# Kernel tuning notes

Hardware: AMD Instinct MI355X
Metric: run time of the kernel (lower is better)

Reference implementation:

```python
import jax, jax.numpy as jnp
import numpy as np

TGT, BSZ, E, H = 2048, 4, 1024, 16
HD = E // H


def setup_inputs() -> dict:
    key = jax.random.key(0)
    ks = jax.random.split(key, 9)
    s = 1.0 / np.sqrt(E)
    return {
        "query": jax.random.normal(ks[0], (TGT, BSZ, E), jnp.float32),
        "wq": jax.random.normal(ks[1], (E, E), jnp.float32) * s,
        "bq": jax.random.normal(ks[2], (E,), jnp.float32) * 0.01,
        "wk": jax.random.normal(ks[3], (E, E), jnp.float32) * s,
        "bk": jax.random.normal(ks[4], (E,), jnp.float32) * 0.01,
        "wv": jax.random.normal(ks[5], (E, E), jnp.float32) * s,
        "bv": jax.random.normal(ks[6], (E,), jnp.float32) * 0.01,
        "wo": jax.random.normal(ks[7], (E, E), jnp.float32) * s,
        "bo": jax.random.normal(ks[8], (E,), jnp.float32) * 0.01,
    }


def reference(query, wq, bq, wk, bk, wv, bv, wo, bo):
    tgt_len, bsz, embed_dim = query.shape
    scaling = HD ** (-0.5)
    # self-attention: q,k,v all projected from query (torch Linear: x @ W.T + b)
    q = (query @ wq.T + bq) * scaling
    k = query @ wk.T + bk
    v = query @ wv.T + bv
    # [T, B, E] -> [B, H, T, HD]
    def split_heads(x):
        return x.reshape(tgt_len, bsz, H, HD).transpose(1, 2, 0, 3)
    qh, kh, vh = split_heads(q), split_heads(k), split_heads(v)
    # attention scores [B, H, Tq, Tk]
    scores = jnp.einsum("bhqd,bhkd->bhqk", qh, kh)
    attn = jax.nn.softmax(scores, axis=-1)
    ctx = jnp.einsum("bhqk,bhkd->bhqd", attn, vh)  # [B, H, T, HD]
    ctx = ctx.transpose(2, 0, 1, 3).reshape(tgt_len, bsz, embed_dim)
    out = ctx @ wo.T + bo
    # need_weights=True default: average attn weights over heads [B, Tq, Tk]
    avg_attn = attn.mean(axis=1)
    return out, avg_attn
```

## Files before the change

kernel.cpp:

```cpp
#include <hip/hip_runtime.h>
#include <cstdint>
#include <cstddef>

typedef _Float16 f16;
typedef f16   f16x4 __attribute__((ext_vector_type(4)));
typedef f16   f16x8 __attribute__((ext_vector_type(8)));
typedef float f32x4 __attribute__((ext_vector_type(4)));

#define MFMA16x32(a, b, c) __builtin_amdgcn_mfma_f32_16x16x32_f16((a), (b), (c), 0, 0, 0)
#define MFMA16x16(a, b, c) __builtin_amdgcn_mfma_f32_16x16x16f16((a), (b), (c), 0, 0, 0)

__device__ __forceinline__ void gload_lds16(const void* g, void* l) {
    __builtin_amdgcn_global_load_lds(
        (const __attribute__((address_space(1))) unsigned int*)g,
        (__attribute__((address_space(3))) unsigned int*)l, 16, 0, 0);
}

__global__ void cvt_f32_f16(const float* __restrict__ in, f16* __restrict__ out, int n8) {
    int i = blockIdx.x * blockDim.x + threadIdx.x;
    if (i >= n8) return;
    const float4 a = ((const float4*)in)[i * 2];
    const float4 b = ((const float4*)in)[i * 2 + 1];
    f16x8 o;
    o[0] = (f16)a.x; o[1] = (f16)a.y; o[2] = (f16)a.z; o[3] = (f16)a.w;
    o[4] = (f16)b.x; o[5] = (f16)b.y; o[6] = (f16)b.z; o[7] = (f16)b.w;
    *(f16x8*)(out + (size_t)i * 8) = o;
}

__global__ __launch_bounds__(256, 3)
void gemm_qkv(const f16* __restrict__ A, const f16* __restrict__ B,
              const float* __restrict__ bq, const float* __restrict__ bk,
              const float* __restrict__ bv,
              f16* __restrict__ q_sp, f16* __restrict__ k_sp, f16* __restrict__ v_sp)
{
    __shared__ f16 Al[128 * 32];
    __shared__ f16 Bl[128 * 32];
    const int tid = threadIdx.x, lane = tid & 63, w = tid >> 6;
    const int wm = w >> 1, wn = w & 1;
    const int m0 = blockIdx.y * 128, n0 = blockIdx.x * 128;
    const int l15 = lane & 15, lh = lane >> 4;

    f32x4 acc[4][4] = {};

    const int c0 = w, c1 = w + 4;
    const int srow0 = c0 * 16 + (lane >> 2);
    const int srow1 = c1 * 16 + (lane >> 2);
    const int scol = (lane & 3) * 8;

    for (int k0 = 0; k0 < 1024; k0 += 32) {
        gload_lds16(A + (size_t)(m0 + srow0) * 1024 + k0 + scol, &Al[c0 * 512]);
        gload_lds16(A + (size_t)(m0 + srow1) * 1024 + k0 + scol, &Al[c1 * 512]);
        gload_lds16(B + (size_t)(n0 + srow0) * 1024 + k0 + scol, &Bl[c0 * 512]);
        gload_lds16(B + (size_t)(n0 + srow1) * 1024 + k0 + scol, &Bl[c1 * 512]);
        __syncthreads();
        f16x8 af[4], bf[4];
        #pragma unroll
        for (int i = 0; i < 4; ++i) {
            af[i] = *(const f16x8*)&Al[(wm * 64 + i * 16 + l15) * 32 + lh * 8];
            bf[i] = *(const f16x8*)&Bl[(wn * 64 + i * 16 + l15) * 32 + lh * 8];
        }
        #pragma unroll
        for (int i = 0; i < 4; ++i)
            #pragma unroll
            for (int j = 0; j < 4; ++j)
                acc[i][j] = MFMA16x32(af[i], bf[j], acc[i][j]);
        __syncthreads();
    }

    const int seg = n0 >> 10;
    const float* bias = (seg == 0) ? bq : (seg == 1) ? bk : bv;
    f16* dst = (seg == 0) ? q_sp : (seg == 1) ? k_sp : v_sp;
    const float scale = (seg == 0) ? 0.18033688011112042f : 1.0f;

    #pragma unroll
    for (int j = 0; j < 4; ++j) {
        const int n = n0 + wn * 64 + j * 16 + l15;
        const int e = n & 1023, hh = e >> 6, d = e & 63;
        const float bsv = bias[e];
        #pragma unroll
        for (int i = 0; i < 4; ++i) {
            #pragma unroll
            for (int r = 0; r < 4; ++r) {
                const int m = m0 + wm * 64 + i * 16 + lh * 4 + r;
                const int t = m >> 2, bb = m & 3;
                dst[((size_t)(bb * 16 + hh) * 2048 + t) * 64 + d] =
                    (f16)((acc[i][j][r] + bsv) * scale);
            }
        }
    }
}

__global__ __launch_bounds__(256)
void vpack(const f16* __restrict__ v_sp, f16* __restrict__ vf_) {
    __shared__ f16 L[16 * 64];
    const int nt = blockIdx.x, bh = blockIdx.y;
    const int tid = threadIdx.x;
    const f16* src = v_sp + ((size_t)bh * 2048 + nt * 16) * 64;
    if (tid < 128)
        *(f16x8*)&L[tid * 8] = *(const f16x8*)&src[tid * 8];
    __syncthreads();
    const int lane = tid >> 2, dt = tid & 3;
    const int l15 = lane & 15, lh = lane >> 4;
    f16x4 o;
    #pragma unroll
    for (int r = 0; r < 4; ++r) o[r] = L[(lh * 4 + r) * 64 + dt * 16 + l15];
    *(f16x4*)&vf_[((size_t)bh * 128 + nt) * 1024 + tid * 4] = o;
}

__global__ __launch_bounds__(512, 2)
void attn_kernel(const f16* __restrict__ q_s, const f16* __restrict__ k_s,
                 const f16* __restrict__ v_f, f16* __restrict__ ctx,
                 float* __restrict__ avg_out)
{
    __shared__ float Oacc[2][1024];
    __shared__ float sumL[8][16];

    const int tid = threadIdx.x;
    const int lane = tid & 63;
    const int w = tid >> 6;
    const int b = blockIdx.y;
    const int t0 = blockIdx.x * 16;
    const int l15 = lane & 15, lh = lane >> 4;

    f16x4 avgv[16] = {};

    Oacc[0][tid] = 0.f; Oacc[0][tid + 512] = 0.f;
    Oacc[1][tid] = 0.f; Oacc[1][tid + 512] = 0.f;

    for (int h = 0; h < 16; ++h) {
        const f16* Qh  = q_s + ((size_t)(b * 16 + h) * 2048 + t0) * 64;
        const f16* Kh  = k_s + (size_t)(b * 16 + h) * 2048 * 64 + (size_t)w * 256 * 64;
        const f16* Vfh = v_f + (size_t)(b * 16 + h) * 131072 + (size_t)w * 16 * 1024;

        const f16x8 qf0 = *(const f16x8*)(Qh + l15 * 64 + lh * 8);
        const f16x8 qf1 = *(const f16x8*)(Qh + l15 * 64 + 32 + lh * 8);

        f16x4 t[16];
        float rsum = 0.f;
        #pragma unroll
        for (int nt = 0; nt < 16; ++nt) {
            const f16* kp = Kh + (size_t)(nt * 16 + l15) * 64 + lh * 8;
            const f16x8 kf0 = *(const f16x8*)(kp);
            const f16x8 kf1 = *(const f16x8*)(kp + 32);
            f32x4 s = {0.f, 0.f, 0.f, 0.f};
            s = MFMA16x32(kf0, qf0, s);
            s = MFMA16x32(kf1, qf1, s);
            const float e0 = __builtin_amdgcn_exp2f(s[0]);
            const float e1 = __builtin_amdgcn_exp2f(s[1]);
            const float e2 = __builtin_amdgcn_exp2f(s[2]);
            const float e3 = __builtin_amdgcn_exp2f(s[3]);
            rsum += (e0 + e1) + (e2 + e3);
            f16x4 tv;
            tv[0] = (f16)e0; tv[1] = (f16)e1; tv[2] = (f16)e2; tv[3] = (f16)e3;
            t[nt] = tv;
        }
        rsum += __shfl_xor(rsum, 16);
        rsum += __shfl_xor(rsum, 32);
        if (lane < 16) sumL[w][lane] = rsum;
        __syncthreads();

        Oacc[(h + 1) & 1][tid] = 0.f;
        Oacc[(h + 1) & 1][tid + 512] = 0.f;

        float total = 0.f;
        #pragma unroll
        for (int ww = 0; ww < 8; ++ww) total += sumL[ww][l15];
        const f16 hinv = (f16)(1.f / total);
        f16x4 hv; hv[0] = hinv; hv[1] = hinv; hv[2] = hinv; hv[3] = hinv;

        f32x4 o0 = {}, o1 = {}, o2 = {}, o3 = {};
        #pragma unroll
        for (int nt = 0; nt < 16; ++nt) {
            const f16x4 tn = t[nt] * hv;
            avgv[nt] += tn;
            const f16* vp = Vfh + nt * 1024 + lane * 16;
            const f16x8 vab = *(const f16x8*)(vp);
            const f16x8 vcd = *(const f16x8*)(vp + 8);
            const f16x4 va = __builtin_shufflevector(vab, vab, 0, 1, 2, 3);
            const f16x4 vb = __builtin_shufflevector(vab, vab, 4, 5, 6, 7);
            const f16x4 vc = __builtin_shufflevector(vcd, vcd, 0, 1, 2, 3);
            const f16x4 vd = __builtin_shufflevector(vcd, vcd, 4, 5, 6, 7);
            o0 = MFMA16x16(tn, va, o0);
            o1 = MFMA16x16(tn, vb, o1);
            o2 = MFMA16x16(tn, vc, o2);
            o3 = MFMA16x16(tn, vd, o3);
        }
        float* Ob = Oacc[h & 1];
        #pragma unroll
        for (int r = 0; r < 4; ++r) {
            const int rowb = (lh * 4 + r) * 64;
            atomicAdd(&Ob[rowb +      l15], o0[r]);
            atomicAdd(&Ob[rowb + 16 + l15], o1[r]);
            atomicAdd(&Ob[rowb + 32 + l15], o2[r]);
            atomicAdd(&Ob[rowb + 48 + l15], o3[r]);
        }
        __syncthreads();

        #pragma unroll
        for (int jj = 0; jj < 2; ++jj) {
            const int idx = tid + jj * 512;
            const int q = idx >> 6, d = idx & 63;
            ctx[((size_t)(t0 + q) * 4 + b) * 1024 + h * 64 + d] = (f16)Ob[idx];
        }
    }

    const float s16 = 1.f / 16.f;
    float* ao = avg_out + ((size_t)b * 2048 + t0 + l15) * 2048 + w * 256 + lh * 4;
    #pragma unroll
    for (int nt = 0; nt < 16; ++nt) {
        float4 v;
        v.x = (float)avgv[nt][0] * s16; v.y = (float)avgv[nt][1] * s16;
        v.z = (float)avgv[nt][2] * s16; v.w = (float)avgv[nt][3] * s16;
        *(float4*)(ao + nt * 16) = v;
    }
}

__global__ __launch_bounds__(256, 3)
void gemm_out(const f16* __restrict__ A, const f16* __restrict__ B,
              const float* __restrict__ bo, float* __restrict__ out)
{
    __shared__ f16 Al[128 * 32];
    __shared__ f16 Bl[128 * 32];
    const int tid = threadIdx.x, lane = tid & 63, w = tid >> 6;
    const int wm = w >> 1, wn = w & 1;
    const int m0 = blockIdx.y * 128, n0 = blockIdx.x * 128;
    const int l15 = lane & 15, lh = lane >> 4;

    f32x4 acc[4][4] = {};
    const int c0 = w, c1 = w + 4;
    const int srow0 = c0 * 16 + (lane >> 2);
    const int srow1 = c1 * 16 + (lane >> 2);
    const int scol = (lane & 3) * 8;

    for (int k0 = 0; k0 < 1024; k0 += 32) {
        gload_lds16(A + (size_t)(m0 + srow0) * 1024 + k0 + scol, &Al[c0 * 512]);
        gload_lds16(A + (size_t)(m0 + srow1) * 1024 + k0 + scol, &Al[c1 * 512]);
        gload_lds16(B + (size_t)(n0 + srow0) * 1024 + k0 + scol, &Bl[c0 * 512]);
        gload_lds16(B + (size_t)(n0 + srow1) * 1024 + k0 + scol, &Bl[c1 * 512]);
        __syncthreads();
        f16x8 af[4], bf[4];
        #pragma unroll
        for (int i = 0; i < 4; ++i) {
            af[i] = *(const f16x8*)&Al[(wm * 64 + i * 16 + l15) * 32 + lh * 8];
            bf[i] = *(const f16x8*)&Bl[(wn * 64 + i * 16 + l15) * 32 + lh * 8];
        }
        #pragma unroll
        for (int i = 0; i < 4; ++i)
            #pragma unroll
            for (int j = 0; j < 4; ++j)
                acc[i][j] = MFMA16x32(af[i], bf[j], acc[i][j]);
        __syncthreads();
    }

    #pragma unroll
    for (int j = 0; j < 4; ++j) {
        const int n = n0 + wn * 64 + j * 16 + l15;
        const float bsv = bo[n];
        #pragma unroll
        for (int i = 0; i < 4; ++i) {
            #pragma unroll
            for (int r = 0; r < 4; ++r) {
                const int m = m0 + wm * 64 + i * 16 + lh * 4 + r;
                out[(size_t)m * 1024 + n] = acc[i][j][r] + bsv;
            }
        }
    }
}

extern "C" void kernel_launch(void* const* d_in, const int* in_sizes, int n_in,
                              void* d_out, int out_size, void* d_ws, size_t ws_size,
                              hipStream_t stream) {
    const float* query = (const float*)d_in[0];
    const float* wq = (const float*)d_in[1];
    const float* bq = (const float*)d_in[2];
    const float* wk = (const float*)d_in[3];
    const float* bk = (const float*)d_in[4];
    const float* wv = (const float*)d_in[5];
    const float* bv = (const float*)d_in[6];
    const float* wo = (const float*)d_in[7];
    const float* bo = (const float*)d_in[8];
    float* out = (float*)d_out;

    f16* wsh  = (f16*)d_ws;
    f16* Xb   = wsh;
    f16* Wqkv = wsh + (8u << 20);
    f16* Wo   = wsh + (11u << 20);
    f16* q_sp = wsh + (12u << 20);
    f16* k_sp = wsh + (20u << 20);
    f16* v_sp = wsh + (28u << 20);
    f16* v_f  = wsh + (36u << 20);
    f16* ctx  = Xb;

    cvt_f32_f16<<<4096, 256, 0, stream>>>(query, Xb, 1048576);
    cvt_f32_f16<<<512, 256, 0, stream>>>(wq, Wqkv, 131072);
    cvt_f32_f16<<<512, 256, 0, stream>>>(wk, Wqkv + (1u << 20), 131072);
    cvt_f32_f16<<<512, 256, 0, stream>>>(wv, Wqkv + (2u << 20), 131072);
    cvt_f32_f16<<<512, 256, 0, stream>>>(wo, Wo, 131072);

    gemm_qkv<<<dim3(24, 64), 256, 0, stream>>>(Xb, Wqkv, bq, bk, bv, q_sp, k_sp, v_sp);
    vpack<<<dim3(128, 64), 256, 0, stream>>>(v_sp, v_f);
    attn_kernel<<<dim3(128, 4), 512, 0, stream>>>(q_sp, k_sp, v_f, ctx,
                                                  out + 8388608 );
    gemm_out<<<dim3(8, 64), 256, 0, stream>>>(ctx, Wo, bo, out);
}
```

Before: 817.1 us.

## Process two 16-query tiles per attention block to reuse K/V loads

```diff
diff --git a/kernel.cpp b/kernel.cpp
--- a/kernel.cpp
+++ b/kernel.cpp
@@ -107,72 +107,89 @@
     *(f16x4*)&vf_[((size_t)bh * 128 + nt) * 1024 + tid * 4] = o;
 }
 
-__global__ __launch_bounds__(512, 2)
+__global__ __launch_bounds__(512, 1)
 void attn_kernel(const f16* __restrict__ q_s, const f16* __restrict__ k_s,
                  const f16* __restrict__ v_f, f16* __restrict__ ctx,
                  float* __restrict__ avg_out)
 {
-    __shared__ float Oacc[2][1024];
-    __shared__ float sumL[8][16];
+    __shared__ float Oacc[2][2][1024];
+    __shared__ float sumL[8][2][16];
 
     const int tid = threadIdx.x;
     const int lane = tid & 63;
     const int w = tid >> 6;
     const int b = blockIdx.y;
-    const int t0 = blockIdx.x * 16;
+    const int t0 = blockIdx.x * 32;
     const int l15 = lane & 15, lh = lane >> 4;
 
-    f16x4 avgv[16] = {};
-
-    Oacc[0][tid] = 0.f; Oacc[0][tid + 512] = 0.f;
-    Oacc[1][tid] = 0.f; Oacc[1][tid + 512] = 0.f;
+    f16x4 avgv0[16] = {}, avgv1[16] = {};
+
+    {
+        float* Oz = &Oacc[0][0][0];
+        #pragma unroll
+        for (int jj = 0; jj < 8; ++jj) Oz[tid + jj * 512] = 0.f;
+    }
+    __syncthreads();
 
     for (int h = 0; h < 16; ++h) {
         const f16* Qh  = q_s + ((size_t)(b * 16 + h) * 2048 + t0) * 64;
         const f16* Kh  = k_s + (size_t)(b * 16 + h) * 2048 * 64 + (size_t)w * 256 * 64;
         const f16* Vfh = v_f + (size_t)(b * 16 + h) * 131072 + (size_t)w * 16 * 1024;
 
-        const f16x8 qf0 = *(const f16x8*)(Qh + l15 * 64 + lh * 8);
-        const f16x8 qf1 = *(const f16x8*)(Qh + l15 * 64 + 32 + lh * 8);
-
-        f16x4 t[16];
-        float rsum = 0.f;
+        const f16x8 qa0 = *(const f16x8*)(Qh + l15 * 64 + lh * 8);
+        const f16x8 qa1 = *(const f16x8*)(Qh + l15 * 64 + 32 + lh * 8);
+        const f16x8 qb0 = *(const f16x8*)(Qh + (16 + l15) * 64 + lh * 8);
+        const f16x8 qb1 = *(const f16x8*)(Qh + (16 + l15) * 64 + 32 + lh * 8);
+
+        f16x4 tA[16], tB[16];
+        float rsA = 0.f, rsB = 0.f;
         #pragma unroll
         for (int nt = 0; nt < 16; ++nt) {
             const f16* kp = Kh + (size_t)(nt * 16 + l15) * 64 + lh * 8;
             const f16x8 kf0 = *(const f16x8*)(kp);
             const f16x8 kf1 = *(const f16x8*)(kp + 32);
-            f32x4 s = {0.f, 0.f, 0.f, 0.f};
-            s = MFMA16x32(kf0, qf0, s);
-            s = MFMA16x32(kf1, qf1, s);
-            const float e0 = __builtin_amdgcn_exp2f(s[0]);
-            const float e1 = __builtin_amdgcn_exp2f(s[1]);
-            const float e2 = __builtin_amdgcn_exp2f(s[2]);
-            const float e3 = __builtin_amdgcn_exp2f(s[3]);
-            rsum += (e0 + e1) + (e2 + e3);
-            f16x4 tv;
-            tv[0] = (f16)e0; tv[1] = (f16)e1; tv[2] = (f16)e2; tv[3] = (f16)e3;
-            t[nt] = tv;
-        }
-        rsum += __shfl_xor(rsum, 16);
-        rsum += __shfl_xor(rsum, 32);
-        if (lane < 16) sumL[w][lane] = rsum;
-        __syncthreads();
-
-        Oacc[(h + 1) & 1][tid] = 0.f;
-        Oacc[(h + 1) & 1][tid + 512] = 0.f;
-
-        float total = 0.f;
-        #pragma unroll
-        for (int ww = 0; ww < 8; ++ww) total += sumL[ww][l15];
-        const f16 hinv = (f16)(1.f / total);
-        f16x4 hv; hv[0] = hinv; hv[1] = hinv; hv[2] = hinv; hv[3] = hinv;
-
-        f32x4 o0 = {}, o1 = {}, o2 = {}, o3 = {};
+            f32x4 sA = {0.f, 0.f, 0.f, 0.f}, sB = {0.f, 0.f, 0.f, 0.f};
+            sA = MFMA16x32(kf0, qa0, sA); sA = MFMA16x32(kf1, qa1, sA);
+            sB = MFMA16x32(kf0, qb0, sB); sB = MFMA16x32(kf1, qb1, sB);
+            f16x4 ta, tb;
+            #pragma unroll
+            for (int r = 0; r < 4; ++r) {
+                const float eA = __builtin_amdgcn_exp2f(sA[r]);
+                const float eB = __builtin_amdgcn_exp2f(sB[r]);
+                rsA += eA; rsB += eB;
+                ta[r] = (f16)eA; tb[r] = (f16)eB;
+            }
+            tA[nt] = ta; tB[nt] = tb;
+        }
+        rsA += __shfl_xor(rsA, 16); rsA += __shfl_xor(rsA, 32);
+        rsB += __shfl_xor(rsB, 16); rsB += __shfl_xor(rsB, 32);
+        if (lane < 16) { sumL[w][0][lane] = rsA; sumL[w][1][lane] = rsB; }
+        __syncthreads();
+
+        {
+            float* Oz = &Oacc[(h + 1) & 1][0][0];
+            #pragma unroll
+            for (int jj = 0; jj < 4; ++jj) Oz[tid + jj * 512] = 0.f;
+        }
+
+        float totA = 0.f, totB = 0.f;
+        #pragma unroll
+        for (int ww = 0; ww < 8; ++ww) {
+            totA += sumL[ww][0][l15];
+            totB += sumL[ww][1][l15];
+        }
+        const f16 hiA = (f16)(1.f / totA), hiB = (f16)(1.f / totB);
+        f16x4 hvA; hvA[0] = hiA; hvA[1] = hiA; hvA[2] = hiA; hvA[3] = hiA;
+        f16x4 hvB; hvB[0] = hiB; hvB[1] = hiB; hvB[2] = hiB; hvB[3] = hiB;
+
+        f32x4 a0 = {}, a1 = {}, a2 = {}, a3 = {};
+        f32x4 b0 = {}, b1 = {}, b2 = {}, b3 = {};
         #pragma unroll
         for (int nt = 0; nt < 16; ++nt) {
-            const f16x4 tn = t[nt] * hv;
-            avgv[nt] += tn;
+            const f16x4 tnA = tA[nt] * hvA;
+            const f16x4 tnB = tB[nt] * hvB;
+            avgv0[nt] += tnA;
+            avgv1[nt] += tnB;
             const f16* vp = Vfh + nt * 1024 + lane * 16;
             const f16x8 vab = *(const f16x8*)(vp);
             const f16x8 vcd = *(const f16x8*)(vp + 8);
@@ -180,38 +197,49 @@
             const f16x4 vb = __builtin_shufflevector(vab, vab, 4, 5, 6, 7);
             const f16x4 vc = __builtin_shufflevector(vcd, vcd, 0, 1, 2, 3);
             const f16x4 vd = __builtin_shufflevector(vcd, vcd, 4, 5, 6, 7);
-            o0 = MFMA16x16(tn, va, o0);
-            o1 = MFMA16x16(tn, vb, o1);
-            o2 = MFMA16x16(tn, vc, o2);
-            o3 = MFMA16x16(tn, vd, o3);
-        }
-        float* Ob = Oacc[h & 1];
+            a0 = MFMA16x16(tnA, va, a0); a1 = MFMA16x16(tnA, vb, a1);
+            a2 = MFMA16x16(tnA, vc, a2); a3 = MFMA16x16(tnA, vd, a3);
+            b0 = MFMA16x16(tnB, va, b0); b1 = MFMA16x16(tnB, vb, b1);
+            b2 = MFMA16x16(tnB, vc, b2); b3 = MFMA16x16(tnB, vd, b3);
+        }
+        float* OA = &Oacc[h & 1][0][0];
+        float* OB = &Oacc[h & 1][1][0];
         #pragma unroll
         for (int r = 0; r < 4; ++r) {
             const int rowb = (lh * 4 + r) * 64;
-            atomicAdd(&Ob[rowb +      l15], o0[r]);
-            atomicAdd(&Ob[rowb + 16 + l15], o1[r]);
-            atomicAdd(&Ob[rowb + 32 + l15], o2[r]);
-            atomicAdd(&Ob[rowb + 48 + l15], o3[r]);
-        }
-        __syncthreads();
-
-        #pragma unroll
-        for (int jj = 0; jj < 2; ++jj) {
+            atomicAdd(&OA[rowb +      l15], a0[r]);
+            atomicAdd(&OA[rowb + 16 + l15], a1[r]);
+            atomicAdd(&OA[rowb + 32 + l15], a2[r]);
+            atomicAdd(&OA[rowb + 48 + l15], a3[r]);
+            atomicAdd(&OB[rowb +      l15], b0[r]);
+            atomicAdd(&OB[rowb + 16 + l15], b1[r]);
+            atomicAdd(&OB[rowb + 32 + l15], b2[r]);
+            atomicAdd(&OB[rowb + 48 + l15], b3[r]);
+        }
+        __syncthreads();
+
+        #pragma unroll
+        for (int jj = 0; jj < 4; ++jj) {
             const int idx = tid + jj * 512;
-            const int q = idx >> 6, d = idx & 63;
-            ctx[((size_t)(t0 + q) * 4 + b) * 1024 + h * 64 + d] = (f16)Ob[idx];
+            const int g = idx >> 10, rem = idx & 1023;
+            const int q = rem >> 6, d = rem & 63;
+            ctx[((size_t)(t0 + g * 16 + q) * 4 + b) * 1024 + h * 64 + d] =
+                (f16)Oacc[h & 1][g][rem];
         }
     }
 
     const float s16 = 1.f / 16.f;
-    float* ao = avg_out + ((size_t)b * 2048 + t0 + l15) * 2048 + w * 256 + lh * 4;
+    float* ao0 = avg_out + ((size_t)b * 2048 + t0 + l15) * 2048 + w * 256 + lh * 4;
+    float* ao1 = avg_out + ((size_t)b * 2048 + t0 + 16 + l15) * 2048 + w * 256 + lh * 4;
     #pragma unroll
     for (int nt = 0; nt < 16; ++nt) {
-        float4 v;
-        v.x = (float)avgv[nt][0] * s16; v.y = (float)avgv[nt][1] * s16;
-        v.z = (float)avgv[nt][2] * s16; v.w = (float)avgv[nt][3] * s16;
-        *(float4*)(ao + nt * 16) = v;
+        float4 v0, v1;
+        v0.x = (float)avgv0[nt][0] * s16; v0.y = (float)avgv0[nt][1] * s16;
+        v0.z = (float)avgv0[nt][2] * s16; v0.w = (float)avgv0[nt][3] * s16;
+        v1.x = (float)avgv1[nt][0] * s16; v1.y = (float)avgv1[nt][1] * s16;
+        v1.z = (float)avgv1[nt][2] * s16; v1.w = (float)avgv1[nt][3] * s16;
+        *(float4*)(ao0 + nt * 16) = v0;
+        *(float4*)(ao1 + nt * 16) = v1;
     }
 }
 
@@ -299,7 +327,7 @@
 
     gemm_qkv<<<dim3(24, 64), 256, 0, stream>>>(Xb, Wqkv, bq, bk, bv, q_sp, k_sp, v_sp);
     vpack<<<dim3(128, 64), 256, 0, stream>>>(v_sp, v_f);
-    attn_kernel<<<dim3(128, 4), 512, 0, stream>>>(q_sp, k_sp, v_f, ctx,
-                                                  out + 8388608 );
+    attn_kernel<<<dim3(64, 4), 512, 0, stream>>>(q_sp, k_sp, v_f, ctx,
+                                                 out + 8388608 );
     gemm_out<<<dim3(8, 64), 256, 0, stream>>>(ctx, Wo, bo, out);
 }
```

Result: faster. 724.4 us (-11.4%).
